# Kernel optimization log

Measured on AMD Instinct MI355X. Metric: run time of the kernel, lower is better.

Reference implementation:

```python
import jax, jax.numpy as jnp
import numpy as np

QMAX = 127.0

def _quantize_int8(x, axis):
    """Symmetric dynamic int8 quantization along `axis`. Returns (int8 values, fp32 scale)."""
    amax = jnp.max(jnp.abs(x), axis=axis, keepdims=True)
    scale = jnp.maximum(amax, 1e-8) / QMAX
    q = jnp.clip(jnp.round(x / scale), -QMAX, QMAX).astype(jnp.int8)
    return q, scale


def setup_inputs() -> dict:
    key = jax.random.key(0)
    kx, kw, kb = jax.random.split(key, 3)
    tokens, d_in, d_out = 4096, 4096, 16384
    x = jax.random.normal(kx, (tokens, d_in), dtype=jnp.float32)
    weight = jax.random.normal(kw, (d_out, d_in), dtype=jnp.float32) * (1.0 / np.sqrt(d_in))
    bias = jax.random.normal(kb, (d_out,), dtype=jnp.float32)
    return {"x": x, "weight": weight, "bias": bias}


def reference(x, weight, bias):
    # Quantize activations per-row (over in_features), weights per-output-column.
    xq, sx = _quantize_int8(x, axis=-1)            # [T, in] int8, [T, 1] scale
    wq, sw = _quantize_int8(weight.T, axis=0)      # [in, out] int8, [1, out] scale
    acc = jnp.matmul(xq, wq, preferred_element_type=jnp.int32)  # [T, out] int32
    out = acc.astype(jnp.float32) * sx * sw + bias
    return out
```

## Files before the change

kernel.cpp:

```cpp
#include <hip/hip_runtime.h>
#include <stdint.h>

typedef int   i32x4 __attribute__((ext_vector_type(4)));
typedef float f32x4 __attribute__((ext_vector_type(4)));

#define AS1 __attribute__((address_space(1)))
#define AS3 __attribute__((address_space(3)))
#define G2L16(gp, lp) __builtin_amdgcn_global_load_lds((const AS1 void*)(gp), (AS3 void*)(lp), 16, 0, 0)

template<int COLS>
__global__ __launch_bounds__(256)
void quant_rows_k(const float* __restrict__ src, int8_t* __restrict__ q,
                  float* __restrict__ scale)
{
    constexpr int PER = COLS / 256;
    static_assert(PER == 16, "pack assumes 16 elems/thread");
    const int row = blockIdx.x;
    const int t   = threadIdx.x;
    const float* s = src + (size_t)row * COLS + (size_t)t * PER;

    float v[PER];
    #pragma unroll
    for (int i = 0; i < PER; i += 4) {
        f32x4 x4 = *reinterpret_cast<const f32x4*>(s + i);
        v[i+0] = x4[0]; v[i+1] = x4[1]; v[i+2] = x4[2]; v[i+3] = x4[3];
    }
    float amax = 0.0f;
    #pragma unroll
    for (int i = 0; i < PER; ++i) amax = fmaxf(amax, fabsf(v[i]));

    #pragma unroll
    for (int off = 32; off > 0; off >>= 1)
        amax = fmaxf(amax, __shfl_xor(amax, off, 64));

    __shared__ float red[4];
    if ((t & 63) == 0) red[t >> 6] = amax;
    __syncthreads();
    amax = fmaxf(fmaxf(red[0], red[1]), fmaxf(red[2], red[3]));

    const float sc = fmaxf(amax, 1e-8f) / 127.0f;
    if (t == 0) scale[row] = sc;

    union { i32x4 v4; int8_t b[16]; } pk;
    #pragma unroll
    for (int i = 0; i < PER; ++i) {
        float r = rintf(v[i] / sc);
        r = fminf(127.0f, fmaxf(-127.0f, r));
        pk.b[i] = (int8_t)r;
    }
    *reinterpret_cast<i32x4*>(q + (size_t)row * COLS + (size_t)t * PER) = pk.v4;
}

#define BM 128
#define BN 128
#define BKB 64

__device__ __forceinline__ i32x4 mfma16(i32x4 a, i32x4 b, i32x4 c) {
    return __builtin_amdgcn_mfma_i32_16x16x64_i8(a, b, c, 0, 0, 0);
}
__device__ __forceinline__ i32x4 ldsld(const int8_t* p) {
    return *reinterpret_cast<const i32x4*>(p);
}
#define FENCE asm volatile("" ::: "memory")
#define BAR   do { FENCE; __builtin_amdgcn_s_barrier(); FENCE; } while (0)

template<bool ST>
__device__ __forceinline__ void tile_fn(
    const int8_t* __restrict__ aB, const int8_t* __restrict__ bB,
    i32x4 (&acc)[4][4],
    const int8_t* __restrict__ gA, const int8_t* __restrict__ gB,
    int8_t* lAn, int8_t* lBn,
    size_t r64, int t16)
{
    if (ST) {
        G2L16(gA,       lAn + t16);
        G2L16(gA + r64, lAn + 4096 + t16);
        G2L16(gB,       lBn + t16);
        G2L16(gB + r64, lBn + 4096 + t16);
    }
    i32x4 a0 = ldsld(aB + 0*1024);
    i32x4 a1 = ldsld(aB + 1*1024);
    i32x4 a2 = ldsld(aB + 2*1024);
    i32x4 a3 = ldsld(aB + 3*1024);
    i32x4 b0 = ldsld(bB + 0*1024);
    i32x4 b1 = ldsld(bB + 1*1024);
    i32x4 b2 = ldsld(bB + 2*1024);
    i32x4 b3 = ldsld(bB + 3*1024);
    acc[0][0] = mfma16(a0, b0, acc[0][0]);
    acc[1][0] = mfma16(a1, b0, acc[1][0]);
    acc[2][0] = mfma16(a2, b0, acc[2][0]);
    acc[3][0] = mfma16(a3, b0, acc[3][0]);
    acc[0][1] = mfma16(a0, b1, acc[0][1]);
    acc[1][1] = mfma16(a1, b1, acc[1][1]);
    acc[2][1] = mfma16(a2, b1, acc[2][1]);
    acc[3][1] = mfma16(a3, b1, acc[3][1]);
    acc[0][2] = mfma16(a0, b2, acc[0][2]);
    acc[1][2] = mfma16(a1, b2, acc[1][2]);
    acc[2][2] = mfma16(a2, b2, acc[2][2]);
    acc[3][2] = mfma16(a3, b2, acc[3][2]);
    acc[0][3] = mfma16(a0, b3, acc[0][3]);
    acc[1][3] = mfma16(a1, b3, acc[1][3]);
    acc[2][3] = mfma16(a2, b3, acc[2][3]);
    acc[3][3] = mfma16(a3, b3, acc[3][3]);
    asm volatile("s_waitcnt vmcnt(0)" ::: "memory");
    BAR;
}

__global__ __launch_bounds__(256, 4)
void gemm_i8_k(const int8_t* __restrict__ A,
               const int8_t* __restrict__ B,
               const float*  __restrict__ sx,
               const float*  __restrict__ sw,
               const float*  __restrict__ bias,
               float* __restrict__ C,
               int M, int N, int K)
{
    __shared__ int8_t lA[2][BM * BKB];
    __shared__ int8_t lB[2][BN * BKB];

    const int t    = threadIdx.x;
    const int lane = t & 63;
    const int wid  = t >> 6;
    const int wm   = wid >> 1;
    const int wn   = wid & 1;

    const int nwg = (int)gridDim.x;
    const int bid = (int)blockIdx.x;
    const int swz = ((nwg & 7) == 0) ? ((bid & 7) * (nwg >> 3) + (bid >> 3)) : bid;
    const int nbn = N / BN;
    const int bm  = swz / nbn;
    const int bn  = swz % nbn;

    const int fr = lane & 15;
    const int c4 = lane >> 4;
    const int kc = ((c4 ^ ((fr >> 1) & 3)) << 4);
    const int aOff = (wm * 64 + fr) * BKB + kc;
    const int bOff = (wn * 64 + fr) * BKB + kc;
    const int8_t* aB0 = &lA[0][aOff];
    const int8_t* aB1 = &lA[1][aOff];
    const int8_t* bB0 = &lB[0][bOff];
    const int8_t* bB1 = &lB[1][bOff];

    const int srow = t >> 2;
    const int scg  = (((t & 3) ^ ((t >> 3) & 3)) << 4);
    const int t16  = t * 16;
    const int8_t* pA = A + (size_t)(bm * BM + srow) * K + scg;
    const int8_t* pB = B + (size_t)(bn * BN + srow) * K + scg;
    const size_t r64 = (size_t)64 * K;

    G2L16(pA,       &lA[0][0]    + t16);
    G2L16(pA + r64, &lA[0][4096] + t16);
    G2L16(pB,       &lB[0][0]    + t16);
    G2L16(pB + r64, &lB[0][4096] + t16);
    asm volatile("s_waitcnt vmcnt(0)" ::: "memory");
    BAR;

    i32x4 acc[4][4] = {};

    const int NT = K / BKB;
    for (int tt = 0; tt + 2 < NT; tt += 2) {
        const size_t ko1 = (size_t)(tt + 1) * BKB;
        tile_fn<true>(aB0, bB0, acc, pA + ko1, pB + ko1, &lA[1][0], &lB[1][0], r64, t16);
        const size_t ko2 = (size_t)(tt + 2) * BKB;
        tile_fn<true>(aB1, bB1, acc, pA + ko2, pB + ko2, &lA[0][0], &lB[0][0], r64, t16);
    }
    {
        const size_t ko1 = (size_t)(NT - 1) * BKB;
        tile_fn<true >(aB0, bB0, acc, pA + ko1, pB + ko1, &lA[1][0], &lB[1][0], r64, t16);
        tile_fn<false>(aB1, bB1, acc, pA, pB, &lA[0][0], &lB[0][0], r64, t16);
    }

    const int r0 = bm * BM + wm * 64 + (c4 << 2);
    const int c0 = bn * BN + wn * 64 + fr;
    #pragma unroll
    for (int ni = 0; ni < 4; ++ni) {
        const int c = c0 + ni * 16;
        const float swc = sw[c];
        const float bc  = bias[c];
        #pragma unroll
        for (int mi = 0; mi < 4; ++mi) {
            const int rb = r0 + mi * 16;
            #pragma unroll
            for (int j = 0; j < 4; ++j) {
                const int r = rb + j;
                C[(size_t)r * N + c] = (float)acc[mi][ni][j] * sx[r] * swc + bc;
            }
        }
    }
}

extern "C" void kernel_launch(void* const* d_in, const int* in_sizes, int n_in,
                              void* d_out, int out_size, void* d_ws, size_t ws_size,
                              hipStream_t stream) {
    const float* x    = (const float*)d_in[0];
    const float* w    = (const float*)d_in[1];
    const float* bias = (const float*)d_in[2];
    float* out = (float*)d_out;

    const int dout   = in_sizes[2];
    const int din    = in_sizes[1] / dout;
    const int tokens = in_sizes[0] / din;

    char* ws = (char*)d_ws;
    float*  sx = (float*)ws;
    float*  sw = (float*)(ws + 16384);
    int8_t* xq = (int8_t*)(ws + 16384 + 65536);
    int8_t* wq = xq + (size_t)tokens * din;

    quant_rows_k<4096><<<tokens, 256, 0, stream>>>(x, xq, sx);
    quant_rows_k<4096><<<dout,   256, 0, stream>>>(w, wq, sw);

    const int grid = (tokens / BM) * (dout / BN);
    gemm_i8_k<<<grid, 256, 0, stream>>>(xq, wq, sx, sw, bias, out, tokens, dout, din);
}
```

Baseline: 497.4 us.

## Enlarge GEMM tile to 256x256 with 8 waves and 4-stage LDS pipeline

Grows the workgroup tile from 128x128 to 256x256 and uses 512 threads, with each wave computing a 128x64 sub-tile so more MFMAs run per LDS fragment load. Replaces the double-buffered LDS with a four-buffer ring that keeps three K-tiles of global-to-LDS loads in flight, waiting with partial vmcnt counts. This aims to cut global/LDS traffic per MFMA and hide load latency. In exchange it uses 64KB of LDS per block, more accumulator registers and lower occupancy, and it needs more careful prologue/epilogue wait counts.

Result: faster. 441.1 us (-11.3%).

```diff
diff --git a/kernel.cpp b/kernel.cpp
--- a/kernel.cpp
+++ b/kernel.cpp
@@ -51,8 +51,8 @@
     *reinterpret_cast<i32x4*>(q + (size_t)row * COLS + (size_t)t * PER) = pk.v4;
 }
 
-#define BM 128
-#define BN 128
+#define BM 256
+#define BN 256
 #define BKB 64
 
 __device__ __forceinline__ i32x4 mfma16(i32x4 a, i32x4 b, i32x4 c) {
@@ -64,49 +64,71 @@
 #define FENCE asm volatile("" ::: "memory")
 #define BAR   do { FENCE; __builtin_amdgcn_s_barrier(); FENCE; } while (0)
 
-template<bool ST>
+template<bool ST, int W>
 __device__ __forceinline__ void tile_fn(
     const int8_t* __restrict__ aB, const int8_t* __restrict__ bB,
-    i32x4 (&acc)[4][4],
+    i32x4 (&acc)[8][4],
     const int8_t* __restrict__ gA, const int8_t* __restrict__ gB,
     int8_t* lAn, int8_t* lBn,
-    size_t r64, int t16)
+    size_t r128, int t16)
 {
     if (ST) {
-        G2L16(gA,       lAn + t16);
-        G2L16(gA + r64, lAn + 4096 + t16);
-        G2L16(gB,       lBn + t16);
-        G2L16(gB + r64, lBn + 4096 + t16);
-    }
+        G2L16(gA,        lAn + t16);
+        G2L16(gA + r128, lAn + 8192 + t16);
+        G2L16(gB,        lBn + t16);
+        G2L16(gB + r128, lBn + 8192 + t16);
+    }
+    i32x4 b0 = ldsld(bB + 0*1024);
+    i32x4 b1 = ldsld(bB + 1*1024);
+    i32x4 b2 = ldsld(bB + 2*1024);
+    i32x4 b3 = ldsld(bB + 3*1024);
     i32x4 a0 = ldsld(aB + 0*1024);
     i32x4 a1 = ldsld(aB + 1*1024);
     i32x4 a2 = ldsld(aB + 2*1024);
     i32x4 a3 = ldsld(aB + 3*1024);
-    i32x4 b0 = ldsld(bB + 0*1024);
-    i32x4 b1 = ldsld(bB + 1*1024);
-    i32x4 b2 = ldsld(bB + 2*1024);
-    i32x4 b3 = ldsld(bB + 3*1024);
+    i32x4 a4 = ldsld(aB + 4*1024);
+    i32x4 a5 = ldsld(aB + 5*1024);
+    i32x4 a6 = ldsld(aB + 6*1024);
+    i32x4 a7 = ldsld(aB + 7*1024);
     acc[0][0] = mfma16(a0, b0, acc[0][0]);
     acc[1][0] = mfma16(a1, b0, acc[1][0]);
     acc[2][0] = mfma16(a2, b0, acc[2][0]);
     acc[3][0] = mfma16(a3, b0, acc[3][0]);
+    acc[4][0] = mfma16(a4, b0, acc[4][0]);
+    acc[5][0] = mfma16(a5, b0, acc[5][0]);
+    acc[6][0] = mfma16(a6, b0, acc[6][0]);
+    acc[7][0] = mfma16(a7, b0, acc[7][0]);
     acc[0][1] = mfma16(a0, b1, acc[0][1]);
     acc[1][1] = mfma16(a1, b1, acc[1][1]);
     acc[2][1] = mfma16(a2, b1, acc[2][1]);
     acc[3][1] = mfma16(a3, b1, acc[3][1]);
+    acc[4][1] = mfma16(a4, b1, acc[4][1]);
+    acc[5][1] = mfma16(a5, b1, acc[5][1]);
+    acc[6][1] = mfma16(a6, b1, acc[6][1]);
+    acc[7][1] = mfma16(a7, b1, acc[7][1]);
     acc[0][2] = mfma16(a0, b2, acc[0][2]);
     acc[1][2] = mfma16(a1, b2, acc[1][2]);
     acc[2][2] = mfma16(a2, b2, acc[2][2]);
     acc[3][2] = mfma16(a3, b2, acc[3][2]);
+    acc[4][2] = mfma16(a4, b2, acc[4][2]);
+    acc[5][2] = mfma16(a5, b2, acc[5][2]);
+    acc[6][2] = mfma16(a6, b2, acc[6][2]);
+    acc[7][2] = mfma16(a7, b2, acc[7][2]);
     acc[0][3] = mfma16(a0, b3, acc[0][3]);
     acc[1][3] = mfma16(a1, b3, acc[1][3]);
     acc[2][3] = mfma16(a2, b3, acc[2][3]);
     acc[3][3] = mfma16(a3, b3, acc[3][3]);
-    asm volatile("s_waitcnt vmcnt(0)" ::: "memory");
-    BAR;
-}
-
-__global__ __launch_bounds__(256, 4)
+    acc[4][3] = mfma16(a4, b3, acc[4][3]);
+    acc[5][3] = mfma16(a5, b3, acc[5][3]);
+    acc[6][3] = mfma16(a6, b3, acc[6][3]);
+    acc[7][3] = mfma16(a7, b3, acc[7][3]);
+    if (W == 8)      asm volatile("s_waitcnt vmcnt(8)" ::: "memory");
+    else if (W == 4) asm volatile("s_waitcnt vmcnt(4)" ::: "memory");
+    else if (W == 0) asm volatile("s_waitcnt vmcnt(0)" ::: "memory");
+    if (W >= 0) BAR;
+}
+
+__global__ __launch_bounds__(512, 2)
 void gemm_i8_k(const int8_t* __restrict__ A,
                const int8_t* __restrict__ B,
                const float*  __restrict__ sx,
@@ -115,14 +137,14 @@
                float* __restrict__ C,
                int M, int N, int K)
 {
-    __shared__ int8_t lA[2][BM * BKB];
-    __shared__ int8_t lB[2][BN * BKB];
+    __shared__ int8_t lA[4][BM * BKB];
+    __shared__ int8_t lB[4][BN * BKB];
 
     const int t    = threadIdx.x;
     const int lane = t & 63;
     const int wid  = t >> 6;
-    const int wm   = wid >> 1;
-    const int wn   = wid & 1;
+    const int wm   = wid >> 2;
+    const int wn   = wid & 3;
 
     const int nwg = (int)gridDim.x;
     const int bid = (int)blockIdx.x;
@@ -134,43 +156,48 @@
     const int fr = lane & 15;
     const int c4 = lane >> 4;
     const int kc = ((c4 ^ ((fr >> 1) & 3)) << 4);
-    const int aOff = (wm * 64 + fr) * BKB + kc;
+    const int aOff = (wm * 128 + fr) * BKB + kc;
     const int bOff = (wn * 64 + fr) * BKB + kc;
-    const int8_t* aB0 = &lA[0][aOff];
-    const int8_t* aB1 = &lA[1][aOff];
-    const int8_t* bB0 = &lB[0][bOff];
-    const int8_t* bB1 = &lB[1][bOff];
+    const int8_t* aF[4] = { &lA[0][aOff], &lA[1][aOff], &lA[2][aOff], &lA[3][aOff] };
+    const int8_t* bF[4] = { &lB[0][bOff], &lB[1][bOff], &lB[2][bOff], &lB[3][bOff] };
+    int8_t* sA[4] = { &lA[0][0], &lA[1][0], &lA[2][0], &lA[3][0] };
+    int8_t* sB[4] = { &lB[0][0], &lB[1][0], &lB[2][0], &lB[3][0] };
 
     const int srow = t >> 2;
     const int scg  = (((t & 3) ^ ((t >> 3) & 3)) << 4);
     const int t16  = t * 16;
     const int8_t* pA = A + (size_t)(bm * BM + srow) * K + scg;
     const int8_t* pB = B + (size_t)(bn * BN + srow) * K + scg;
-    const size_t r64 = (size_t)64 * K;
-
-    G2L16(pA,       &lA[0][0]    + t16);
-    G2L16(pA + r64, &lA[0][4096] + t16);
-    G2L16(pB,       &lB[0][0]    + t16);
-    G2L16(pB + r64, &lB[0][4096] + t16);
-    asm volatile("s_waitcnt vmcnt(0)" ::: "memory");
+    const size_t r128 = (size_t)128 * K;
+
+    #pragma unroll
+    for (int tau = 0; tau < 3; ++tau) {
+        const size_t ko = (size_t)tau * BKB;
+        G2L16(pA + ko,        sA[tau] + t16);
+        G2L16(pA + ko + r128, sA[tau] + 8192 + t16);
+        G2L16(pB + ko,        sB[tau] + t16);
+        G2L16(pB + ko + r128, sB[tau] + 8192 + t16);
+    }
+    asm volatile("s_waitcnt vmcnt(8)" ::: "memory");
     BAR;
 
-    i32x4 acc[4][4] = {};
+    i32x4 acc[8][4] = {};
 
     const int NT = K / BKB;
-    for (int tt = 0; tt + 2 < NT; tt += 2) {
-        const size_t ko1 = (size_t)(tt + 1) * BKB;
-        tile_fn<true>(aB0, bB0, acc, pA + ko1, pB + ko1, &lA[1][0], &lB[1][0], r64, t16);
-        const size_t ko2 = (size_t)(tt + 2) * BKB;
-        tile_fn<true>(aB1, bB1, acc, pA + ko2, pB + ko2, &lA[0][0], &lB[0][0], r64, t16);
+    for (int tt = 0; tt < NT - 4; tt += 4) {
+        tile_fn<true, 8>(aF[0], bF[0], acc, pA + (size_t)(tt + 3) * BKB, pB + (size_t)(tt + 3) * BKB, sA[3], sB[3], r128, t16);
+        tile_fn<true, 8>(aF[1], bF[1], acc, pA + (size_t)(tt + 4) * BKB, pB + (size_t)(tt + 4) * BKB, sA[0], sB[0], r128, t16);
+        tile_fn<true, 8>(aF[2], bF[2], acc, pA + (size_t)(tt + 5) * BKB, pB + (size_t)(tt + 5) * BKB, sA[1], sB[1], r128, t16);
+        tile_fn<true, 8>(aF[3], bF[3], acc, pA + (size_t)(tt + 6) * BKB, pB + (size_t)(tt + 6) * BKB, sA[2], sB[2], r128, t16);
     }
     {
-        const size_t ko1 = (size_t)(NT - 1) * BKB;
-        tile_fn<true >(aB0, bB0, acc, pA + ko1, pB + ko1, &lA[1][0], &lB[1][0], r64, t16);
-        tile_fn<false>(aB1, bB1, acc, pA, pB, &lA[0][0], &lB[0][0], r64, t16);
-    }
-
-    const int r0 = bm * BM + wm * 64 + (c4 << 2);
+        tile_fn<true,  8>(aF[0], bF[0], acc, pA + (size_t)(NT - 1) * BKB, pB + (size_t)(NT - 1) * BKB, sA[3], sB[3], r128, t16);
+        tile_fn<false, 4>(aF[1], bF[1], acc, pA, pB, sA[0], sB[0], r128, t16);
+        tile_fn<false, 0>(aF[2], bF[2], acc, pA, pB, sA[1], sB[1], r128, t16);
+        tile_fn<false,-1>(aF[3], bF[3], acc, pA, pB, sA[2], sB[2], r128, t16);
+    }
+
+    const int r0 = bm * BM + wm * 128 + (c4 << 2);
     const int c0 = bn * BN + wn * 64 + fr;
     #pragma unroll
     for (int ni = 0; ni < 4; ++ni) {
@@ -178,7 +205,7 @@
         const float swc = sw[c];
         const float bc  = bias[c];
         #pragma unroll
-        for (int mi = 0; mi < 4; ++mi) {
+        for (int mi = 0; mi < 8; ++mi) {
             const int rb = r0 + mi * 16;
             #pragma unroll
             for (int j = 0; j < 4; ++j) {
@@ -211,5 +238,5 @@
     quant_rows_k<4096><<<dout,   256, 0, stream>>>(w, wq, sw);
 
     const int grid = (tokens / BM) * (dout / BN);
-    gemm_i8_k<<<grid, 256, 0, stream>>>(xq, wq, sx, sw, bias, out, tokens, dout, din);
-}
+    gemm_i8_k<<<grid, 512, 0, stream>>>(xq, wq, sx, sw, bias, out, tokens, dout, din);
+}
```

## Enlarge GEMM tiles to 256x256x128 with 32x32 int8 MFMA and phased loads

Applied to the files above, without the earlier changes.

Replaces the 128x128x64 tile GEMM with 256x256 output tiles, a K-step of 128 and 512 threads (8 waves), switching from 16x16x64 to 32x32x32 int8 MFMA instructions. The main loop is split into four phases that interleave LDS reads, partial global-to-LDS prefetches and MFMA bursts, using setprio, sched_barrier and partial vmcnt waits. The larger tiles are meant to raise arithmetic intensity and cut global and LDS traffic per MFMA. In exchange, LDS use grows to 128KB per block, occupancy drops, the barrier count rises, and the layout and waitcnt choreography become more fragile.

Measured after the change: 509.2 us. 1.02x slower.

```diff
diff --git a/kernel.cpp b/kernel.cpp
--- a/kernel.cpp
+++ b/kernel.cpp
@@ -1,8 +1,9 @@
 #include <hip/hip_runtime.h>
 #include <stdint.h>
 
-typedef int   i32x4 __attribute__((ext_vector_type(4)));
-typedef float f32x4 __attribute__((ext_vector_type(4)));
+typedef int   i32x4  __attribute__((ext_vector_type(4)));
+typedef int   i32x16 __attribute__((ext_vector_type(16)));
+typedef float f32x4  __attribute__((ext_vector_type(4)));
 
 #define AS1 __attribute__((address_space(1)))
 #define AS3 __attribute__((address_space(3)))
@@ -51,62 +52,124 @@
     *reinterpret_cast<i32x4*>(q + (size_t)row * COLS + (size_t)t * PER) = pk.v4;
 }
 
-#define BM 128
-#define BN 128
-#define BKB 64
-
-__device__ __forceinline__ i32x4 mfma16(i32x4 a, i32x4 b, i32x4 c) {
-    return __builtin_amdgcn_mfma_i32_16x16x64_i8(a, b, c, 0, 0, 0);
+#define BM 256
+#define BN 256
+#define BKB 128
+
+__device__ __forceinline__ i32x16 mfma32(i32x4 a, i32x4 b, i32x16 c) {
+    return __builtin_amdgcn_mfma_i32_32x32x32_i8(a, b, c, 0, 0, 0);
 }
 __device__ __forceinline__ i32x4 ldsld(const int8_t* p) {
     return *reinterpret_cast<const i32x4*>(p);
 }
 #define FENCE asm volatile("" ::: "memory")
 #define BAR   do { FENCE; __builtin_amdgcn_s_barrier(); FENCE; } while (0)
+#define LGKM0 asm volatile("s_waitcnt lgkmcnt(0)" ::: "memory")
+#define SCHB  __builtin_amdgcn_sched_barrier(0)
 
 template<bool ST>
 __device__ __forceinline__ void tile_fn(
-    const int8_t* __restrict__ aB, const int8_t* __restrict__ bB,
-    i32x4 (&acc)[4][4],
+    const int8_t* __restrict__ aP, const int8_t* __restrict__ bP,
+    i32x16 (&acc)[4][2],
     const int8_t* __restrict__ gA, const int8_t* __restrict__ gB,
     int8_t* lAn, int8_t* lBn,
-    size_t r64, int t16)
+    size_t r128, int t16)
 {
-    if (ST) {
-        G2L16(gA,       lAn + t16);
-        G2L16(gA + r64, lAn + 4096 + t16);
-        G2L16(gB,       lBn + t16);
-        G2L16(gB + r64, lBn + 4096 + t16);
-    }
-    i32x4 a0 = ldsld(aB + 0*1024);
-    i32x4 a1 = ldsld(aB + 1*1024);
-    i32x4 a2 = ldsld(aB + 2*1024);
-    i32x4 a3 = ldsld(aB + 3*1024);
-    i32x4 b0 = ldsld(bB + 0*1024);
-    i32x4 b1 = ldsld(bB + 1*1024);
-    i32x4 b2 = ldsld(bB + 2*1024);
-    i32x4 b3 = ldsld(bB + 3*1024);
-    acc[0][0] = mfma16(a0, b0, acc[0][0]);
-    acc[1][0] = mfma16(a1, b0, acc[1][0]);
-    acc[2][0] = mfma16(a2, b0, acc[2][0]);
-    acc[3][0] = mfma16(a3, b0, acc[3][0]);
-    acc[0][1] = mfma16(a0, b1, acc[0][1]);
-    acc[1][1] = mfma16(a1, b1, acc[1][1]);
-    acc[2][1] = mfma16(a2, b1, acc[2][1]);
-    acc[3][1] = mfma16(a3, b1, acc[3][1]);
-    acc[0][2] = mfma16(a0, b2, acc[0][2]);
-    acc[1][2] = mfma16(a1, b2, acc[1][2]);
-    acc[2][2] = mfma16(a2, b2, acc[2][2]);
-    acc[3][2] = mfma16(a3, b2, acc[3][2]);
-    acc[0][3] = mfma16(a0, b3, acc[0][3]);
-    acc[1][3] = mfma16(a1, b3, acc[1][3]);
-    acc[2][3] = mfma16(a2, b3, acc[2][3]);
-    acc[3][3] = mfma16(a3, b3, acc[3][3]);
-    asm volatile("s_waitcnt vmcnt(0)" ::: "memory");
-    BAR;
-}
-
-__global__ __launch_bounds__(256, 4)
+    i32x4 a00 = ldsld(aP + 0);
+    i32x4 a01 = ldsld(aP + 1024);
+    i32x4 a10 = ldsld(aP + 2048);
+    i32x4 a11 = ldsld(aP + 3072);
+    i32x4 b00 = ldsld(bP + 0);
+    i32x4 b01 = ldsld(bP + 1024);
+    i32x4 b10 = ldsld(bP + 2048);
+    i32x4 b11 = ldsld(bP + 3072);
+    if (ST) {
+        G2L16(gB,        lBn + t16);
+        G2L16(gB + r128, lBn + 8192 + t16);
+    }
+    BAR; LGKM0; SCHB;
+    __builtin_amdgcn_s_setprio(1);
+    acc[0][0] = mfma32(a00, b00, acc[0][0]);
+    acc[1][0] = mfma32(a10, b00, acc[1][0]);
+    acc[0][1] = mfma32(a00, b10, acc[0][1]);
+    acc[1][1] = mfma32(a10, b10, acc[1][1]);
+    acc[0][0] = mfma32(a01, b01, acc[0][0]);
+    acc[1][0] = mfma32(a11, b01, acc[1][0]);
+    acc[0][1] = mfma32(a01, b11, acc[0][1]);
+    acc[1][1] = mfma32(a11, b11, acc[1][1]);
+    __builtin_amdgcn_s_setprio(0);
+    BAR;
+    i32x4 a20 = ldsld(aP + 4096);
+    i32x4 a21 = ldsld(aP + 5120);
+    i32x4 a30 = ldsld(aP + 6144);
+    i32x4 a31 = ldsld(aP + 7168);
+    if (ST) {
+        G2L16(gB + 64,        lBn + 16384 + t16);
+        G2L16(gB + r128 + 64, lBn + 24576 + t16);
+    }
+    BAR; LGKM0; SCHB;
+    __builtin_amdgcn_s_setprio(1);
+    acc[2][0] = mfma32(a20, b00, acc[2][0]);
+    acc[3][0] = mfma32(a30, b00, acc[3][0]);
+    acc[2][1] = mfma32(a20, b10, acc[2][1]);
+    acc[3][1] = mfma32(a30, b10, acc[3][1]);
+    acc[2][0] = mfma32(a21, b01, acc[2][0]);
+    acc[3][0] = mfma32(a31, b01, acc[3][0]);
+    acc[2][1] = mfma32(a21, b11, acc[2][1]);
+    acc[3][1] = mfma32(a31, b11, acc[3][1]);
+    __builtin_amdgcn_s_setprio(0);
+    if (ST) asm volatile("s_waitcnt vmcnt(4)" ::: "memory");
+    else    asm volatile("s_waitcnt vmcnt(0)" ::: "memory");
+    BAR;
+    i32x4 c00 = ldsld(aP + 16384);
+    i32x4 c01 = ldsld(aP + 17408);
+    i32x4 c10 = ldsld(aP + 18432);
+    i32x4 c11 = ldsld(aP + 19456);
+    i32x4 d00 = ldsld(bP + 16384);
+    i32x4 d01 = ldsld(bP + 17408);
+    i32x4 d10 = ldsld(bP + 18432);
+    i32x4 d11 = ldsld(bP + 19456);
+    if (ST) {
+        G2L16(gA,        lAn + t16);
+        G2L16(gA + r128, lAn + 8192 + t16);
+    }
+    BAR; LGKM0; SCHB;
+    __builtin_amdgcn_s_setprio(1);
+    acc[0][0] = mfma32(c00, d00, acc[0][0]);
+    acc[1][0] = mfma32(c10, d00, acc[1][0]);
+    acc[0][1] = mfma32(c00, d10, acc[0][1]);
+    acc[1][1] = mfma32(c10, d10, acc[1][1]);
+    acc[0][0] = mfma32(c01, d01, acc[0][0]);
+    acc[1][0] = mfma32(c11, d01, acc[1][0]);
+    acc[0][1] = mfma32(c01, d11, acc[0][1]);
+    acc[1][1] = mfma32(c11, d11, acc[1][1]);
+    __builtin_amdgcn_s_setprio(0);
+    BAR;
+    i32x4 e00 = ldsld(aP + 20480);
+    i32x4 e01 = ldsld(aP + 21504);
+    i32x4 e10 = ldsld(aP + 22528);
+    i32x4 e11 = ldsld(aP + 23552);
+    if (ST) {
+        G2L16(gA + 64,        lAn + 16384 + t16);
+        G2L16(gA + r128 + 64, lAn + 24576 + t16);
+    }
+    BAR; LGKM0; SCHB;
+    __builtin_amdgcn_s_setprio(1);
+    acc[2][0] = mfma32(e00, d00, acc[2][0]);
+    acc[3][0] = mfma32(e10, d00, acc[3][0]);
+    acc[2][1] = mfma32(e00, d10, acc[2][1]);
+    acc[3][1] = mfma32(e10, d10, acc[3][1]);
+    acc[2][0] = mfma32(e01, d01, acc[2][0]);
+    acc[3][0] = mfma32(e11, d01, acc[3][0]);
+    acc[2][1] = mfma32(e01, d11, acc[2][1]);
+    acc[3][1] = mfma32(e11, d11, acc[3][1]);
+    __builtin_amdgcn_s_setprio(0);
+    if (ST) asm volatile("s_waitcnt vmcnt(2)" ::: "memory");
+    else    asm volatile("s_waitcnt vmcnt(0)" ::: "memory");
+    BAR;
+}
+
+__global__ __launch_bounds__(512, 2)
 void gemm_i8_k(const int8_t* __restrict__ A,
                const int8_t* __restrict__ B,
                const float*  __restrict__ sx,
@@ -115,14 +178,14 @@
                float* __restrict__ C,
                int M, int N, int K)
 {
-    __shared__ int8_t lA[2][BM * BKB];
-    __shared__ int8_t lB[2][BN * BKB];
+    __shared__ int8_t lA[2][32768];
+    __shared__ int8_t lB[2][32768];
 
     const int t    = threadIdx.x;
     const int lane = t & 63;
     const int wid  = t >> 6;
-    const int wm   = wid >> 1;
-    const int wn   = wid & 1;
+    const int wm   = wid >> 2;
+    const int wn   = wid & 3;
 
     const int nwg = (int)gridDim.x;
     const int bid = (int)blockIdx.x;
@@ -131,59 +194,58 @@
     const int bm  = swz / nbn;
     const int bn  = swz % nbn;
 
-    const int fr = lane & 15;
-    const int c4 = lane >> 4;
-    const int kc = ((c4 ^ ((fr >> 1) & 3)) << 4);
-    const int aOff = (wm * 64 + fr) * BKB + kc;
-    const int bOff = (wn * 64 + fr) * BKB + kc;
-    const int8_t* aB0 = &lA[0][aOff];
-    const int8_t* aB1 = &lA[1][aOff];
-    const int8_t* bB0 = &lB[0][bOff];
-    const int8_t* bB1 = &lB[1][bOff];
-
-    const int srow = t >> 2;
-    const int scg  = (((t & 3) ^ ((t >> 3) & 3)) << 4);
-    const int t16  = t * 16;
-    const int8_t* pA = A + (size_t)(bm * BM + srow) * K + scg;
-    const int8_t* pB = B + (size_t)(bn * BN + srow) * K + scg;
-    const size_t r64 = (size_t)64 * K;
-
-    G2L16(pA,       &lA[0][0]    + t16);
-    G2L16(pA + r64, &lA[0][4096] + t16);
-    G2L16(pB,       &lB[0][0]    + t16);
-    G2L16(pB + r64, &lB[0][4096] + t16);
-    asm volatile("s_waitcnt vmcnt(0)" ::: "memory");
-    BAR;
-
-    i32x4 acc[4][4] = {};
+    const int8_t* aP0 = &lA[0][wm * 8192 + lane * 16];
+    const int8_t* aP1 = &lA[1][wm * 8192 + lane * 16];
+    const int8_t* bP0 = &lB[0][(wn >> 1) * 8192 + (wn & 1) * 4096 + lane * 16];
+    const int8_t* bP1 = &lB[1][(wn >> 1) * 8192 + (wn & 1) * 4096 + lane * 16];
+
+    const int rS = ((t >> 7) * 32) + (t & 31);
+    const int kS = ((t >> 6) & 1) * 32 + ((t >> 5) & 1) * 16;
+    const int t16 = t * 16;
+    const int8_t* pA = A + (size_t)(bm * BM + rS) * K + kS;
+    const int8_t* pB = B + (size_t)(bn * BN + rS) * K + kS;
+    const size_t r128 = (size_t)128 * K;
+
+    G2L16(pB,              &lB[0][0]     + t16);
+    G2L16(pB + r128,       &lB[0][8192]  + t16);
+    G2L16(pB + 64,         &lB[0][16384] + t16);
+    G2L16(pB + r128 + 64,  &lB[0][24576] + t16);
+    G2L16(pA,              &lA[0][0]     + t16);
+    G2L16(pA + r128,       &lA[0][8192]  + t16);
+    G2L16(pA + 64,         &lA[0][16384] + t16);
+    G2L16(pA + r128 + 64,  &lA[0][24576] + t16);
+    asm volatile("s_waitcnt vmcnt(2)" ::: "memory");
+    BAR;
+
+    i32x16 acc[4][2] = {};
 
     const int NT = K / BKB;
     for (int tt = 0; tt + 2 < NT; tt += 2) {
         const size_t ko1 = (size_t)(tt + 1) * BKB;
-        tile_fn<true>(aB0, bB0, acc, pA + ko1, pB + ko1, &lA[1][0], &lB[1][0], r64, t16);
+        tile_fn<true>(aP0, bP0, acc, pA + ko1, pB + ko1, &lA[1][0], &lB[1][0], r128, t16);
         const size_t ko2 = (size_t)(tt + 2) * BKB;
-        tile_fn<true>(aB1, bB1, acc, pA + ko2, pB + ko2, &lA[0][0], &lB[0][0], r64, t16);
+        tile_fn<true>(aP1, bP1, acc, pA + ko2, pB + ko2, &lA[0][0], &lB[0][0], r128, t16);
     }
     {
         const size_t ko1 = (size_t)(NT - 1) * BKB;
-        tile_fn<true >(aB0, bB0, acc, pA + ko1, pB + ko1, &lA[1][0], &lB[1][0], r64, t16);
-        tile_fn<false>(aB1, bB1, acc, pA, pB, &lA[0][0], &lB[0][0], r64, t16);
-    }
-
-    const int r0 = bm * BM + wm * 64 + (c4 << 2);
-    const int c0 = bn * BN + wn * 64 + fr;
-    #pragma unroll
-    for (int ni = 0; ni < 4; ++ni) {
-        const int c = c0 + ni * 16;
+        tile_fn<true >(aP0, bP0, acc, pA + ko1, pB + ko1, &lA[1][0], &lB[1][0], r128, t16);
+        tile_fn<false>(aP1, bP1, acc, pA, pB, &lA[0][0], &lB[0][0], r128, t16);
+    }
+
+    const int hi   = lane >> 5;
+    const int col0 = bn * BN + wn * 64 + (lane & 31);
+    #pragma unroll
+    for (int ni = 0; ni < 2; ++ni) {
+        const int c = col0 + ni * 32;
         const float swc = sw[c];
         const float bc  = bias[c];
         #pragma unroll
         for (int mi = 0; mi < 4; ++mi) {
-            const int rb = r0 + mi * 16;
+            const int rb = bm * BM + wm * 128 + mi * 32 + 4 * hi;
             #pragma unroll
-            for (int j = 0; j < 4; ++j) {
-                const int r = rb + j;
-                C[(size_t)r * N + c] = (float)acc[mi][ni][j] * sx[r] * swc + bc;
+            for (int r = 0; r < 16; ++r) {
+                const int row = rb + (r & 3) + 8 * (r >> 2);
+                C[(size_t)row * N + c] = (float)acc[mi][ni][r] * sx[row] * swc + bc;
             }
         }
     }
@@ -211,5 +273,5 @@
     quant_rows_k<4096><<<dout,   256, 0, stream>>>(w, wq, sw);
 
     const int grid = (tokens / BM) * (dout / BN);
-    gemm_i8_k<<<grid, 256, 0, stream>>>(xq, wq, sx, sw, bias, out, tokens, dout, din);
-}
+    gemm_i8_k<<<grid, 512, 0, stream>>>(xq, wq, sx, sw, bias, out, tokens, dout, din);
+}
```
